# Kernel optimization log

Measured on AMD Instinct MI355X. Metric: run time of the kernel, lower is better.

Reference implementation:

```python
import jax, jax.numpy as jnp
import numpy as np

EPS_NORM = 1e-12   # torch F.normalize eps
EPS_TRIP = 1e-6    # torch pairwise_distance eps
MARGIN = 1.0

def _l2_normalize(x, axis=1):
    n = jnp.linalg.norm(x, axis=axis, keepdims=True)
    return x / jnp.maximum(n, EPS_NORM)

def setup_inputs() -> dict:
    key = jax.random.key(0)
    k1, k2 = jax.random.split(key)
    bs, m, d = 32768, 2048, 256
    query = jax.random.normal(k1, (bs, d), dtype=jnp.float32)
    memory = jax.random.normal(k2, (m, d), dtype=jnp.float32)
    return {"query": query, "memory": memory}

def reference(query, memory):
    m, d = memory.shape
    q = _l2_normalize(query, axis=1)                      # [bs, d]
    score = jnp.matmul(q, memory.T)                       # [bs, m]
    sfx_score_query = jax.nn.softmax(score, axis=0)       # softmax over batch
    sfx_score_memory = jax.nn.softmax(score, axis=1)      # softmax over slots

    # --- update (note: original passes sfx_score_query for BOTH score args) ---
    max_idx = jnp.argmax(sfx_score_query, axis=1)         # [bs] topk(k=1) over dim=1
    colmax = jnp.max(sfx_score_query, axis=0)             # [m]
    sel = jnp.take_along_axis(sfx_score_query, max_idx[:, None], axis=1)[:, 0]  # score[j, max_idx[j]]
    w = sel / colmax[max_idx]                              # [bs]
    # vectorized form of the per-slot gather/weighted-sum loop (segment-sum)
    query_update = jax.ops.segment_sum(w[:, None] * q, max_idx, num_segments=m)  # [m, d]
    updated_memory = jax.lax.stop_gradient(_l2_normalize(query_update + memory, axis=1))

    # --- read (uses ORIGINAL memory in the train path) ---
    concat_memory = jnp.matmul(jax.lax.stop_gradient(sfx_score_memory), memory)  # [bs, d]
    update_query = jnp.concatenate([q, concat_memory], axis=1)                   # [bs, 2d]

    # --- losses (computed from sfx_score_memory as intended) ---
    top2_vals, top2_idx = jax.lax.top_k(sfx_score_memory, 2)
    pos = jax.lax.stop_gradient(memory[top2_idx[:, 0]])   # [bs, d]
    neg = jax.lax.stop_gradient(memory[top2_idx[:, 1]])   # [bs, d]
    gathering_loss = jnp.mean((q - pos) ** 2)
    d_pos = jnp.linalg.norm(q - pos + EPS_TRIP, axis=1)
    d_neg = jnp.linalg.norm(q - neg + EPS_TRIP, axis=1)
    spreading_loss = jnp.mean(jnp.maximum(d_pos - d_neg + MARGIN, 0.0))

    return (update_query, updated_memory, sfx_score_query, sfx_score_memory,
            gathering_loss, spreading_loss)
```

## Files before the change

kernel.cpp:

```cpp
#include <hip/hip_runtime.h>
#include <hip/hip_bf16.h>
#include <cstddef>
#include <cstdint>

#define BS 32768
#define MSLOT 2048
#define D 256
#define NCHUNK 256

typedef _Float16 f16;
typedef _Float16 f16x8 __attribute__((ext_vector_type(8)));
typedef float f32x4 __attribute__((ext_vector_type(4)));

__device__ __forceinline__ void lds_cp16(void* dst, const void* src) {
    __builtin_amdgcn_global_load_lds(
        (const __attribute__((address_space(1))) void*)src,
        (__attribute__((address_space(3))) void*)dst, 16, 0, 0);
}

__device__ __forceinline__ void top2_merge(float& a0, int& ai0, float& a1, int& ai1,
                                           float b0, int bi0, float b1, int bi1)
{
    bool bt = (b0 > a0) || (b0 == a0 && bi0 < ai0);
    float n0, n1; int ni0, ni1;
    if (bt) {
        n0 = b0; ni0 = bi0;
        bool s2 = (b1 > a0) || (b1 == a0 && bi1 < ai0);
        n1 = s2 ? b1 : a0; ni1 = s2 ? bi1 : ai0;
    } else {
        n0 = a0; ni0 = ai0;
        bool s2 = (b0 > a1) || (b0 == a1 && bi0 < ai1);
        n1 = s2 ? b0 : a1; ni1 = s2 ? bi0 : ai1;
    }
    a0 = n0; ai0 = ni0; a1 = n1; ai1 = ni1;
}

__global__ __launch_bounds__(256) void k_prepq(const float* __restrict__ query,
                                               float* __restrict__ out0,
                                               f16* __restrict__ qh, f16* __restrict__ ql)
{
    __shared__ float sbuf[4];
    const int i = blockIdx.x, t = threadIdx.x;
    float v = query[(size_t)i * D + t];
    float ss = v * v;
#pragma unroll
    for (int off = 32; off; off >>= 1) ss += __shfl_xor(ss, off, 64);
    if ((t & 63) == 0) sbuf[t >> 6] = ss;
    __syncthreads();
    float tot = (sbuf[0] + sbuf[1]) + (sbuf[2] + sbuf[3]);
    float n = fmaxf(sqrtf(tot), 1e-12f);
    float qv = v / n;
    out0[(size_t)i * (2 * D) + t] = qv;
    float qs = qv * 256.0f;
    f16 h = (f16)qs;
    f16 lo = (f16)(qs - (float)h);
    qh[(size_t)i * D + t] = h;
    ql[(size_t)i * D + t] = lo;
}

__global__ __launch_bounds__(256) void k_prepm(const float* __restrict__ memory,
                                               f16* __restrict__ mh, f16* __restrict__ ml,
                                               f16* __restrict__ memT)
{
    const int j = blockIdx.x, t = threadIdx.x;
    float m = memory[(size_t)j * D + t];
    f16 h = (f16)m;
    f16 lo = (f16)(m - (float)h);
    mh[(size_t)j * D + t] = h;
    ml[(size_t)j * D + t] = lo;
    memT[(size_t)t * MSLOT + j] = h;
}

__global__ __launch_bounds__(256) void k_score(const f16* __restrict__ qh, const f16* __restrict__ ql,
                                               const f16* __restrict__ mh, const f16* __restrict__ ml,
                                               float* __restrict__ out2,
                                               float* __restrict__ colpart)
{
    __shared__ __align__(16) f16 Ah[4096], Al[4096], Bh[4096], Bl[4096];
    __shared__ float sepM[4][4][16], sepS[4][4][16];
    const int t = threadIdx.x;
    const int l = t & 63, w = t >> 6;
    const int wr = w >> 1, wc = w & 1;
    const int lk = l >> 4, lm = l & 15;
    const int i0 = blockIdx.y * 128, j0 = blockIdx.x * 128;

    f32x4 acc[4][4] = {};

    for (int ks = 0; ks < 8; ++ks) {
        const int k0 = ks * 32;
#pragma unroll
        for (int c = 0; c < 2; ++c) {
            int s = c * 256 + t;
            int r = s >> 2, cc = s & 3;
            int scc = cc ^ ((r >> 1) & 3);
            size_t aoff = (size_t)(i0 + r) * D + k0 + scc * 8;
            size_t boff = (size_t)(j0 + r) * D + k0 + scc * 8;
            lds_cp16(&Ah[s * 8], qh + aoff);
            lds_cp16(&Al[s * 8], ql + aoff);
            lds_cp16(&Bh[s * 8], mh + boff);
            lds_cp16(&Bl[s * 8], ml + boff);
        }
        __syncthreads();
        f16x8 a_h[4], a_l[4], b_h[4], b_l[4];
#pragma unroll
        for (int m = 0; m < 4; ++m) {
            int r = wr * 64 + m * 16 + lm;
            int off = r * 64 + ((lk ^ ((r >> 1) & 3)) << 4);
            a_h[m] = *(const f16x8*)((const char*)Ah + off);
            a_l[m] = *(const f16x8*)((const char*)Al + off);
        }
#pragma unroll
        for (int n = 0; n < 4; ++n) {
            int r = wc * 64 + n * 16 + lm;
            int off = r * 64 + ((lk ^ ((r >> 1) & 3)) << 4);
            b_h[n] = *(const f16x8*)((const char*)Bh + off);
            b_l[n] = *(const f16x8*)((const char*)Bl + off);
        }
#pragma unroll
        for (int m = 0; m < 4; ++m)
#pragma unroll
            for (int n = 0; n < 4; ++n) {
                acc[m][n] = __builtin_amdgcn_mfma_f32_16x16x32_f16(a_h[m], b_h[n], acc[m][n], 0, 0, 0);
                acc[m][n] = __builtin_amdgcn_mfma_f32_16x16x32_f16(a_h[m], b_l[n], acc[m][n], 0, 0, 0);
                acc[m][n] = __builtin_amdgcn_mfma_f32_16x16x32_f16(a_l[m], b_h[n], acc[m][n], 0, 0, 0);
            }
        __syncthreads();
    }

    const float sc = 1.0f / 256.0f;
#pragma unroll
    for (int m = 0; m < 4; ++m)
#pragma unroll
        for (int n = 0; n < 4; ++n)
            acc[m][n] *= sc;

#pragma unroll
    for (int m = 0; m < 4; ++m) {
        int row = i0 + wr * 64 + m * 16 + lk * 4;
#pragma unroll
        for (int n = 0; n < 4; ++n) {
            int col = j0 + wc * 64 + n * 16 + lm;
#pragma unroll
            for (int r = 0; r < 4; ++r)
                out2[(size_t)(row + r) * MSLOT + col] = acc[m][n][r];
        }
    }

    float cm[4], cs[4];
#pragma unroll
    for (int n = 0; n < 4; ++n) {
        float mx = -INFINITY;
#pragma unroll
        for (int m = 0; m < 4; ++m)
#pragma unroll
            for (int r = 0; r < 4; ++r) mx = fmaxf(mx, acc[m][n][r]);
        float sm = 0.0f;
#pragma unroll
        for (int m = 0; m < 4; ++m)
#pragma unroll
            for (int r = 0; r < 4; ++r) sm += __expf(acc[m][n][r] - mx);
#pragma unroll
        for (int off = 16; off <= 32; off <<= 1) {
            float om = __shfl_xor(mx, off, 64);
            float os = __shfl_xor(sm, off, 64);
            float nm = fmaxf(mx, om);
            sm = sm * __expf(mx - nm) + os * __expf(om - nm);
            mx = nm;
        }
        cm[n] = mx; cs[n] = sm;
    }
    if (l < 16) {
#pragma unroll
        for (int n = 0; n < 4; ++n) { sepM[w][n][l] = cm[n]; sepS[w][n][l] = cs[n]; }
    }
    __syncthreads();
    if (w < 2 && l < 16) {
#pragma unroll
        for (int n = 0; n < 4; ++n) {
            float m1 = sepM[w][n][l], s1 = sepS[w][n][l];
            float m2 = sepM[w + 2][n][l], s2 = sepS[w + 2][n][l];
            float nm = fmaxf(m1, m2);
            float ns = s1 * __expf(m1 - nm) + s2 * __expf(m2 - nm);
            int col = j0 + w * 64 + n * 16 + l;
            size_t o = ((size_t)blockIdx.y * MSLOT + col) * 2;
            colpart[o + 0] = nm;
            colpart[o + 1] = ns;
        }
    }
}

__global__ __launch_bounds__(256) void k_colmerge(const float* __restrict__ colpart,
                                                  float* __restrict__ colM,
                                                  float* __restrict__ colSinv,
                                                  float* __restrict__ colC)
{
    const int col = blockIdx.x * 256 + threadIdx.x;
    float m = -INFINITY, s = 0.0f;
    for (int c = 0; c < NCHUNK; ++c) {
        size_t o = ((size_t)c * MSLOT + col) * 2;
        float pm = colpart[o + 0], ps = colpart[o + 1];
        float nm = fmaxf(m, pm);
        s = s * __expf(m - nm) + ps * __expf(pm - nm);
        m = nm;
    }
    colM[col] = m;
    colSinv[col] = 1.0f / s;
    colC[col] = m + __logf(s);
}

__global__ __launch_bounds__(256) void k_rowtrans(float* __restrict__ sq,
                                                  float* __restrict__ sm,
                                                  const float* __restrict__ colM,
                                                  const float* __restrict__ colSinv,
                                                  const float* __restrict__ colC,
                                                  const float* __restrict__ out0,
                                                  const float* __restrict__ memory,
                                                  int* __restrict__ jstarA, float* __restrict__ wA,
                                                  float* __restrict__ gpart, float* __restrict__ spart)
{
    __shared__ float swm[4], sws[4];
    __shared__ float st0v[4], st1v[4]; __shared__ int st0i[4], st1i[4];
    __shared__ float sav[4], sar[4];  __shared__ int sai[4];
    __shared__ float sg[4], sdp[4], sdn[4];

    const int i = blockIdx.x, t = threadIdx.x;
    const int l = t & 63, w = t >> 6;
    float* row = sq + (size_t)i * MSLOT;
    float v[8];
#pragma unroll
    for (int k = 0; k < 8; ++k) v[k] = row[t + k * 256];

    float lmx = v[0];
#pragma unroll
    for (int k = 1; k < 8; ++k) lmx = fmaxf(lmx, v[k]);
#pragma unroll
    for (int off = 32; off; off >>= 1) lmx = fmaxf(lmx, __shfl_xor(lmx, off, 64));
    if (l == 0) swm[w] = lmx;
    __syncthreads();
    const float rm = fmaxf(fmaxf(swm[0], swm[1]), fmaxf(swm[2], swm[3]));

    float ls = 0.0f;
#pragma unroll
    for (int k = 0; k < 8; ++k) ls += __expf(v[k] - rm);

    float v0 = -INFINITY, v1 = -INFINITY; int i0 = 0x7fffffff, i1 = 0x7fffffff;
#pragma unroll
    for (int k = 0; k < 8; ++k) {
        int idx = t + k * 256; float cv = v[k];
        if (cv > v0)      { v1 = v0; i1 = i0; v0 = cv; i0 = idx; }
        else if (cv > v1) { v1 = cv; i1 = idx; }
    }

    float av = -INFINITY, araw = 0.0f; int ai = 0x7fffffff;
#pragma unroll
    for (int k = 0; k < 8; ++k) {
        int idx = t + k * 256;
        float x = v[k] - colC[idx];
        if (x > av || (x == av && idx < ai)) { av = x; ai = idx; araw = v[k]; }
    }

#pragma unroll
    for (int off = 32; off; off >>= 1) ls += __shfl_xor(ls, off, 64);
#pragma unroll
    for (int off = 1; off < 64; off <<= 1) {
        float b0 = __shfl_xor(v0, off, 64), b1 = __shfl_xor(v1, off, 64);
        int  bi0 = __shfl_xor(i0, off, 64), bi1 = __shfl_xor(i1, off, 64);
        top2_merge(v0, i0, v1, i1, b0, bi0, b1, bi1);
    }
#pragma unroll
    for (int off = 1; off < 64; off <<= 1) {
        float ov = __shfl_xor(av, off, 64), oraw = __shfl_xor(araw, off, 64);
        int   oi = __shfl_xor(ai, off, 64);
        if (ov > av || (ov == av && oi < ai)) { av = ov; ai = oi; araw = oraw; }
    }
    if (l == 0) {
        sws[w] = ls;
        st0v[w] = v0; st0i[w] = i0; st1v[w] = v1; st1i[w] = i1;
        sav[w] = av; sai[w] = ai; sar[w] = araw;
    }
    __syncthreads();

    const float rs = (sws[0] + sws[1]) + (sws[2] + sws[3]);
    const float rsinv = 1.0f / rs;

    float T0 = -INFINITY, T1 = -INFINITY; int I0 = 0x7fffffff, I1 = 0x7fffffff;
#pragma unroll
    for (int ww = 0; ww < 4; ++ww)
        top2_merge(T0, I0, T1, I1, st0v[ww], st0i[ww], st1v[ww], st1i[ww]);

    float AV = -INFINITY, AR = 0.0f; int AI = 0x7fffffff;
#pragma unroll
    for (int ww = 0; ww < 4; ++ww) {
        if (sav[ww] > AV || (sav[ww] == AV && sai[ww] < AI)) { AV = sav[ww]; AI = sai[ww]; AR = sar[ww]; }
    }

    float qv = out0[(size_t)i * (2 * D) + t];
    float pv = memory[(size_t)I0 * D + t];
    float nv = memory[(size_t)I1 * D + t];
    float dq = qv - pv;
    float g  = dq * dq;
    float dp = dq + 1e-6f;          dp *= dp;
    float dn = (qv - nv) + 1e-6f;   dn *= dn;
#pragma unroll
    for (int off = 32; off; off >>= 1) {
        g  += __shfl_xor(g, off, 64);
        dp += __shfl_xor(dp, off, 64);
        dn += __shfl_xor(dn, off, 64);
    }
    if (l == 0) { sg[w] = g; sdp[w] = dp; sdn[w] = dn; }
    __syncthreads();
    if (t == 0) {
        float gs  = (sg[0] + sg[1]) + (sg[2] + sg[3]);
        float dps = (sdp[0] + sdp[1]) + (sdp[2] + sdp[3]);
        float dns = (sdn[0] + sdn[1]) + (sdn[2] + sdn[3]);
        gpart[i] = gs;
        spart[i] = fmaxf(sqrtf(dps) - sqrtf(dns) + 1.0f, 0.0f);
        jstarA[i] = AI;
        wA[i] = __expf(AR - colM[AI]);
    }

#pragma unroll
    for (int k = 0; k < 8; ++k) {
        int j = t + k * 256;
        row[j] = __expf(v[k] - colM[j]) * colSinv[j];
        sm[(size_t)i * MSLOT + j] = __expf(v[k] - rm) * rsinv;
    }
}

__global__ __launch_bounds__(256) void k_scatter(const float* __restrict__ out0,
                                                 const int* __restrict__ jstarA,
                                                 const float* __restrict__ wA,
                                                 float* __restrict__ qupd)
{
    const int i = blockIdx.x, t = threadIdx.x;
    const int j = jstarA[i];
    const float wv = wA[i];
    unsafeAtomicAdd(&qupd[(size_t)j * D + t], wv * out0[(size_t)i * (2 * D) + t]);
}

__global__ __launch_bounds__(256) void k_updmem(const float* __restrict__ qupd,
                                                const float* __restrict__ memory,
                                                float* __restrict__ out1)
{
    __shared__ float sbuf[4];
    const int j = blockIdx.x, t = threadIdx.x;
    float v = qupd[(size_t)j * D + t] + memory[(size_t)j * D + t];
    float ss = v * v;
#pragma unroll
    for (int off = 32; off; off >>= 1) ss += __shfl_xor(ss, off, 64);
    if ((t & 63) == 0) sbuf[t >> 6] = ss;
    __syncthreads();
    float tot = (sbuf[0] + sbuf[1]) + (sbuf[2] + sbuf[3]);
    float n = fmaxf(sqrtf(tot), 1e-12f);
    out1[(size_t)j * D + t] = v / n;
}

__global__ __launch_bounds__(256) void k_concat(const float* __restrict__ P,
                                                const f16* __restrict__ memT,
                                                float* __restrict__ out0)
{
    __shared__ __align__(16) f16 As[2][4096 / 2];
    __shared__ __align__(16) f16 Bs[2][8192];
    const int t = threadIdx.x;
    const int l = t & 63, w = t >> 6;
    const int lk = l >> 4, lm = l & 15;
    const int i0 = blockIdx.x * 64;

    const int ar = t >> 2, acm = t & 3;
    const int aslot = acm ^ ((ar >> 1) & 3);

    f32x4 acc[4][4] = {};
    float4 pa, pb;

    {
        const float4* ap = (const float4*)(P + (size_t)(i0 + ar) * MSLOT + acm * 8);
        pa = ap[0]; pb = ap[1];
#pragma unroll
        for (int c = 0; c < 4; ++c) {
            int s = c * 256 + t;
            int n = s >> 2, cc = s & 3;
            int scc = cc ^ ((n >> 1) & 3);
            lds_cp16(&Bs[0][s * 8], memT + (size_t)n * MSLOT + scc * 8);
        }
        f16x8 h;
        h[0] = (f16)pa.x; h[1] = (f16)pa.y; h[2] = (f16)pa.z; h[3] = (f16)pa.w;
        h[4] = (f16)pb.x; h[5] = (f16)pb.y; h[6] = (f16)pb.z; h[7] = (f16)pb.w;
        *(f16x8*)((char*)As[0] + ar * 64 + (aslot << 4)) = h;
        __syncthreads();
    }

    for (int ks = 0; ks < 64; ++ks) {
        const int cur = ks & 1, nxt = cur ^ 1;
        if (ks < 63) {
            const int k0 = (ks + 1) * 32;
            const float4* ap = (const float4*)(P + (size_t)(i0 + ar) * MSLOT + k0 + acm * 8);
            pa = ap[0]; pb = ap[1];
#pragma unroll
            for (int c = 0; c < 4; ++c) {
                int s = c * 256 + t;
                int n = s >> 2, cc = s & 3;
                int scc = cc ^ ((n >> 1) & 3);
                lds_cp16(&Bs[nxt][s * 8], memT + (size_t)n * MSLOT + k0 + scc * 8);
            }
        }
        f16x8 af[4], bf[4];
#pragma unroll
        for (int m = 0; m < 4; ++m) {
            int r = m * 16 + lm;
            int off = r * 64 + ((lk ^ ((r >> 1) & 3)) << 4);
            af[m] = *(const f16x8*)((const char*)As[cur] + off);
        }
#pragma unroll
        for (int n = 0; n < 4; ++n) {
            int r = w * 64 + n * 16 + lm;
            int off = r * 64 + ((lk ^ ((r >> 1) & 3)) << 4);
            bf[n] = *(const f16x8*)((const char*)Bs[cur] + off);
        }
#pragma unroll
        for (int m = 0; m < 4; ++m)
#pragma unroll
            for (int n = 0; n < 4; ++n)
                acc[m][n] = __builtin_amdgcn_mfma_f32_16x16x32_f16(af[m], bf[n], acc[m][n], 0, 0, 0);

        if (ks < 63) {
            f16x8 h;
            h[0] = (f16)pa.x; h[1] = (f16)pa.y; h[2] = (f16)pa.z; h[3] = (f16)pa.w;
            h[4] = (f16)pb.x; h[5] = (f16)pb.y; h[6] = (f16)pb.z; h[7] = (f16)pb.w;
            *(f16x8*)((char*)As[nxt] + ar * 64 + (aslot << 4)) = h;
        }
        __syncthreads();
    }

#pragma unroll
    for (int m = 0; m < 4; ++m) {
        int row = i0 + m * 16 + lk * 4;
#pragma unroll
        for (int n = 0; n < 4; ++n) {
            int col = w * 64 + n * 16 + lm;
#pragma unroll
            for (int r = 0; r < 4; ++r)
                out0[(size_t)(row + r) * (2 * D) + D + col] = acc[m][n][r];
        }
    }
}

__global__ __launch_bounds__(256) void k_losses(const float* __restrict__ gpart,
                                                const float* __restrict__ spart,
                                                float* __restrict__ out45)
{
    __shared__ float sf[256];
    const int t = threadIdx.x;
    float g = 0.f, s = 0.f;
    for (int i = t; i < BS; i += 256) { g += gpart[i]; s += spart[i]; }
    sf[t] = g; __syncthreads();
    for (int off = 128; off; off >>= 1) { if (t < off) sf[t] += sf[t + off]; __syncthreads(); }
    float gt = sf[0]; __syncthreads();
    sf[t] = s; __syncthreads();
    for (int off = 128; off; off >>= 1) { if (t < off) sf[t] += sf[t + off]; __syncthreads(); }
    float st = sf[0];
    if (t == 0) {
        out45[0] = gt / (float)((size_t)BS * D);
        out45[1] = st / (float)BS;
    }
}

extern "C" void kernel_launch(void* const* d_in, const int* in_sizes, int n_in,
                              void* d_out, int out_size, void* d_ws, size_t ws_size,
                              hipStream_t stream)
{
    const float* query  = (const float*)d_in[0];
    const float* memory = (const float*)d_in[1];

    float* out  = (float*)d_out;
    float* out0 = out;
    float* out1 = out0 + (size_t)BS * 2 * D;
    float* out2 = out1 + (size_t)MSLOT * D;
    float* out3 = out2 + (size_t)BS * MSLOT;
    float* out45 = out3 + (size_t)BS * MSLOT;

    f16* qh   = (f16*)d_ws;
    f16* ql   = qh + (size_t)BS * D;
    f16* mh   = ql + (size_t)BS * D;
    f16* ml   = mh + (size_t)MSLOT * D;
    f16* memT = ml + (size_t)MSLOT * D;
    float* colpart = (float*)(memT + (size_t)D * MSLOT);
    float* colM    = colpart + (size_t)NCHUNK * MSLOT * 2;
    float* colSinv = colM + MSLOT;
    float* colC    = colSinv + MSLOT;
    float* wA      = colC + MSLOT;
    int*   jstarA  = (int*)(wA + BS);
    float* gpart   = (float*)(jstarA + BS);
    float* spart   = gpart + BS;
    float* qupd    = spart + BS;

    k_prepq<<<BS, 256, 0, stream>>>(query, out0, qh, ql);
    k_prepm<<<MSLOT, 256, 0, stream>>>(memory, mh, ml, memT);

    k_score<<<dim3(MSLOT / 128, BS / 128), 256, 0, stream>>>(qh, ql, mh, ml, out2, colpart);

    k_colmerge<<<MSLOT / 256, 256, 0, stream>>>(colpart, colM, colSinv, colC);

    k_rowtrans<<<BS, 256, 0, stream>>>(out2, out3, colM, colSinv, colC, out0, memory,
                                       jstarA, wA, gpart, spart);

    hipMemsetAsync(qupd, 0, (size_t)MSLOT * D * sizeof(float), stream);
    k_scatter<<<BS, 256, 0, stream>>>(out0, jstarA, wA, qupd);
    k_updmem<<<MSLOT, 256, 0, stream>>>(qupd, memory, out1);

    k_concat<<<BS / 64, 256, 0, stream>>>(out3, memT, out0);

    k_losses<<<1, 256, 0, stream>>>(gpart, spart, out45);
}
```

Measured before the change: 612.4 us.

## Double-buffer score GEMM, vectorize rowtrans, emit f16 probs for concat GEMM

Double-buffers the LDS tiles in the score GEMM so global loads overlap MFMA work. Vectorizes k_rowtrans loads and stores with a contiguous per-thread column layout and makes it also write an f16 copy of the row softmax. k_concat then reads that copy directly via LDS async copies, with a 128-row tile. The qupd memset is folded into k_prepm, and k_scatter reads the f16 hi/lo query halves instead of the fp32 output. The extra f16 probability buffer adds write traffic and workspace, and argmax tie-breaking now relies on ascending index order within each thread.

```diff
diff --git a/kernel.cpp b/kernel.cpp
--- a/kernel.cpp
+++ b/kernel.cpp
@@ -60,7 +60,8 @@
 
 __global__ __launch_bounds__(256) void k_prepm(const float* __restrict__ memory,
                                                f16* __restrict__ mh, f16* __restrict__ ml,
-                                               f16* __restrict__ memT)
+                                               f16* __restrict__ memT,
+                                               float* __restrict__ qupd)
 {
     const int j = blockIdx.x, t = threadIdx.x;
     float m = memory[(size_t)j * D + t];
@@ -69,6 +70,7 @@
     mh[(size_t)j * D + t] = h;
     ml[(size_t)j * D + t] = lo;
     memT[(size_t)t * MSLOT + j] = h;
+    qupd[(size_t)j * D + t] = 0.0f;
 }
 
 __global__ __launch_bounds__(256) void k_score(const f16* __restrict__ qh, const f16* __restrict__ ql,
@@ -76,7 +78,7 @@
                                                float* __restrict__ out2,
                                                float* __restrict__ colpart)
 {
-    __shared__ __align__(16) f16 Ah[4096], Al[4096], Bh[4096], Bl[4096];
+    __shared__ __align__(16) f16 Ah[2][4096], Al[2][4096], Bh[2][4096], Bl[2][4096];
     __shared__ float sepM[4][4][16], sepS[4][4][16];
     const int t = threadIdx.x;
     const int l = t & 63, w = t >> 6;
@@ -86,35 +88,43 @@
 
     f32x4 acc[4][4] = {};
 
+#define STAGE_SCORE(buf, k0)                                                     \
+    {                                                                            \
+        _Pragma("unroll")                                                        \
+        for (int c = 0; c < 2; ++c) {                                            \
+            int s = c * 256 + t;                                                 \
+            int r = s >> 2, cc = s & 3;                                          \
+            int scc = cc ^ ((r >> 1) & 3);                                       \
+            size_t aoff = (size_t)(i0 + r) * D + (k0) + scc * 8;                 \
+            size_t boff = (size_t)(j0 + r) * D + (k0) + scc * 8;                 \
+            lds_cp16(&Ah[buf][s * 8], qh + aoff);                                \
+            lds_cp16(&Al[buf][s * 8], ql + aoff);                                \
+            lds_cp16(&Bh[buf][s * 8], mh + boff);                                \
+            lds_cp16(&Bl[buf][s * 8], ml + boff);                                \
+        }                                                                        \
+    }
+
+    STAGE_SCORE(0, 0);
+    __syncthreads();
+
     for (int ks = 0; ks < 8; ++ks) {
-        const int k0 = ks * 32;
-#pragma unroll
-        for (int c = 0; c < 2; ++c) {
-            int s = c * 256 + t;
-            int r = s >> 2, cc = s & 3;
-            int scc = cc ^ ((r >> 1) & 3);
-            size_t aoff = (size_t)(i0 + r) * D + k0 + scc * 8;
-            size_t boff = (size_t)(j0 + r) * D + k0 + scc * 8;
-            lds_cp16(&Ah[s * 8], qh + aoff);
-            lds_cp16(&Al[s * 8], ql + aoff);
-            lds_cp16(&Bh[s * 8], mh + boff);
-            lds_cp16(&Bl[s * 8], ml + boff);
-        }
-        __syncthreads();
+        const int cur = ks & 1;
+        if (ks < 7) STAGE_SCORE(cur ^ 1, (ks + 1) * 32);
+
         f16x8 a_h[4], a_l[4], b_h[4], b_l[4];
 #pragma unroll
         for (int m = 0; m < 4; ++m) {
             int r = wr * 64 + m * 16 + lm;
             int off = r * 64 + ((lk ^ ((r >> 1) & 3)) << 4);
-            a_h[m] = *(const f16x8*)((const char*)Ah + off);
-            a_l[m] = *(const f16x8*)((const char*)Al + off);
+            a_h[m] = *(const f16x8*)((const char*)Ah[cur] + off);
+            a_l[m] = *(const f16x8*)((const char*)Al[cur] + off);
         }
 #pragma unroll
         for (int n = 0; n < 4; ++n) {
             int r = wc * 64 + n * 16 + lm;
             int off = r * 64 + ((lk ^ ((r >> 1) & 3)) << 4);
-            b_h[n] = *(const f16x8*)((const char*)Bh + off);
-            b_l[n] = *(const f16x8*)((const char*)Bl + off);
+            b_h[n] = *(const f16x8*)((const char*)Bh[cur] + off);
+            b_l[n] = *(const f16x8*)((const char*)Bl[cur] + off);
         }
 #pragma unroll
         for (int m = 0; m < 4; ++m)
@@ -126,6 +136,7 @@
             }
         __syncthreads();
     }
+#undef STAGE_SCORE
 
     const float sc = 1.0f / 256.0f;
 #pragma unroll
@@ -210,6 +221,7 @@
 
 __global__ __launch_bounds__(256) void k_rowtrans(float* __restrict__ sq,
                                                   float* __restrict__ sm,
+                                                  f16* __restrict__ pf16,
                                                   const float* __restrict__ colM,
                                                   const float* __restrict__ colSinv,
                                                   const float* __restrict__ colC,
@@ -225,10 +237,29 @@
 
     const int i = blockIdx.x, t = threadIdx.x;
     const int l = t & 63, w = t >> 6;
+    const int jb = t * 8;
     float* row = sq + (size_t)i * MSLOT;
+
     float v[8];
-#pragma unroll
-    for (int k = 0; k < 8; ++k) v[k] = row[t + k * 256];
+    {
+        float4 va = *(const float4*)(row + jb);
+        float4 vb = *(const float4*)(row + jb + 4);
+        v[0] = va.x; v[1] = va.y; v[2] = va.z; v[3] = va.w;
+        v[4] = vb.x; v[5] = vb.y; v[6] = vb.z; v[7] = vb.w;
+    }
+    float cCv[8], cMv[8], cSv[8];
+    {
+        float4 a = *(const float4*)(colC + jb);
+        float4 b = *(const float4*)(colC + jb + 4);
+        cCv[0] = a.x; cCv[1] = a.y; cCv[2] = a.z; cCv[3] = a.w;
+        cCv[4] = b.x; cCv[5] = b.y; cCv[6] = b.z; cCv[7] = b.w;
+        a = *(const float4*)(colM + jb); b = *(const float4*)(colM + jb + 4);
+        cMv[0] = a.x; cMv[1] = a.y; cMv[2] = a.z; cMv[3] = a.w;
+        cMv[4] = b.x; cMv[5] = b.y; cMv[6] = b.z; cMv[7] = b.w;
+        a = *(const float4*)(colSinv + jb); b = *(const float4*)(colSinv + jb + 4);
+        cSv[0] = a.x; cSv[1] = a.y; cSv[2] = a.z; cSv[3] = a.w;
+        cSv[4] = b.x; cSv[5] = b.y; cSv[6] = b.z; cSv[7] = b.w;
+    }
 
     float lmx = v[0];
 #pragma unroll
@@ -246,7 +277,7 @@
     float v0 = -INFINITY, v1 = -INFINITY; int i0 = 0x7fffffff, i1 = 0x7fffffff;
 #pragma unroll
     for (int k = 0; k < 8; ++k) {
-        int idx = t + k * 256; float cv = v[k];
+        int idx = jb + k; float cv = v[k];
         if (cv > v0)      { v1 = v0; i1 = i0; v0 = cv; i0 = idx; }
         else if (cv > v1) { v1 = cv; i1 = idx; }
     }
@@ -254,9 +285,9 @@
     float av = -INFINITY, araw = 0.0f; int ai = 0x7fffffff;
 #pragma unroll
     for (int k = 0; k < 8; ++k) {
-        int idx = t + k * 256;
-        float x = v[k] - colC[idx];
-        if (x > av || (x == av && idx < ai)) { av = x; ai = idx; araw = v[k]; }
+        int idx = jb + k;
+        float x = v[k] - cCv[k];
+        if (x > av) { av = x; ai = idx; araw = v[k]; }
     }
 
 #pragma unroll
@@ -319,23 +350,35 @@
         wA[i] = __expf(AR - colM[AI]);
     }
 
+    float oq[8], om[8];
 #pragma unroll
     for (int k = 0; k < 8; ++k) {
-        int j = t + k * 256;
-        row[j] = __expf(v[k] - colM[j]) * colSinv[j];
-        sm[(size_t)i * MSLOT + j] = __expf(v[k] - rm) * rsinv;
-    }
-}
-
-__global__ __launch_bounds__(256) void k_scatter(const float* __restrict__ out0,
+        oq[k] = __expf(v[k] - cMv[k]) * cSv[k];
+        om[k] = __expf(v[k] - rm) * rsinv;
+    }
+    float4 q0 = {oq[0], oq[1], oq[2], oq[3]}, q1 = {oq[4], oq[5], oq[6], oq[7]};
+    float4 m0 = {om[0], om[1], om[2], om[3]}, m1 = {om[4], om[5], om[6], om[7]};
+    *(float4*)(row + jb) = q0;
+    *(float4*)(row + jb + 4) = q1;
+    *(float4*)(sm + (size_t)i * MSLOT + jb) = m0;
+    *(float4*)(sm + (size_t)i * MSLOT + jb + 4) = m1;
+    f16x8 h;
+#pragma unroll
+    for (int k = 0; k < 8; ++k) h[k] = (f16)om[k];
+    *(f16x8*)(pf16 + (size_t)i * MSLOT + jb) = h;
+}
+
+__global__ __launch_bounds__(256) void k_scatter(const f16* __restrict__ qh,
+                                                 const f16* __restrict__ ql,
                                                  const int* __restrict__ jstarA,
                                                  const float* __restrict__ wA,
                                                  float* __restrict__ qupd)
 {
     const int i = blockIdx.x, t = threadIdx.x;
     const int j = jstarA[i];
-    const float wv = wA[i];
-    unsafeAtomicAdd(&qupd[(size_t)j * D + t], wv * out0[(size_t)i * (2 * D) + t]);
+    const float wv = wA[i] * (1.0f / 256.0f);
+    float qv = (float)qh[(size_t)i * D + t] + (float)ql[(size_t)i * D + t];
+    unsafeAtomicAdd(&qupd[(size_t)j * D + t], wv * qv);
 }
 
 __global__ __launch_bounds__(256) void k_updmem(const float* __restrict__ qupd,
@@ -355,88 +398,75 @@
     out1[(size_t)j * D + t] = v / n;
 }
 
-__global__ __launch_bounds__(256) void k_concat(const float* __restrict__ P,
+__global__ __launch_bounds__(256) void k_concat(const f16* __restrict__ P,
                                                 const f16* __restrict__ memT,
                                                 float* __restrict__ out0)
 {
-    __shared__ __align__(16) f16 As[2][4096 / 2];
+    __shared__ __align__(16) f16 As[2][4096];
     __shared__ __align__(16) f16 Bs[2][8192];
     const int t = threadIdx.x;
     const int l = t & 63, w = t >> 6;
     const int lk = l >> 4, lm = l & 15;
-    const int i0 = blockIdx.x * 64;
-
-    const int ar = t >> 2, acm = t & 3;
-    const int aslot = acm ^ ((ar >> 1) & 3);
-
-    f32x4 acc[4][4] = {};
-    float4 pa, pb;
-
-    {
-        const float4* ap = (const float4*)(P + (size_t)(i0 + ar) * MSLOT + acm * 8);
-        pa = ap[0]; pb = ap[1];
-#pragma unroll
-        for (int c = 0; c < 4; ++c) {
-            int s = c * 256 + t;
-            int n = s >> 2, cc = s & 3;
-            int scc = cc ^ ((n >> 1) & 3);
-            lds_cp16(&Bs[0][s * 8], memT + (size_t)n * MSLOT + scc * 8);
-        }
-        f16x8 h;
-        h[0] = (f16)pa.x; h[1] = (f16)pa.y; h[2] = (f16)pa.z; h[3] = (f16)pa.w;
-        h[4] = (f16)pb.x; h[5] = (f16)pb.y; h[6] = (f16)pb.z; h[7] = (f16)pb.w;
-        *(f16x8*)((char*)As[0] + ar * 64 + (aslot << 4)) = h;
-        __syncthreads();
-    }
+    const int i0 = blockIdx.x * 128;
+
+#define STAGE_CC(buf, k0)                                                        \
+    {                                                                            \
+        _Pragma("unroll")                                                        \
+        for (int c = 0; c < 2; ++c) {                                            \
+            int s = c * 256 + t;                                                 \
+            int r = s >> 2, cc = s & 3;                                          \
+            int scc = cc ^ ((r >> 1) & 3);                                       \
+            lds_cp16(&As[buf][s * 8], P + (size_t)(i0 + r) * MSLOT + (k0) + scc * 8); \
+        }                                                                        \
+        _Pragma("unroll")                                                        \
+        for (int c = 0; c < 4; ++c) {                                            \
+            int s = c * 256 + t;                                                 \
+            int n = s >> 2, cc = s & 3;                                          \
+            int scc = cc ^ ((n >> 1) & 3);                                       \
+            lds_cp16(&Bs[buf][s * 8], memT + (size_t)n * MSLOT + (k0) + scc * 8); \
+        }                                                                        \
+    }
+
+    f32x4 acc[2][16] = {};
+    STAGE_CC(0, 0);
+    __syncthreads();
 
     for (int ks = 0; ks < 64; ++ks) {
-        const int cur = ks & 1, nxt = cur ^ 1;
-        if (ks < 63) {
-            const int k0 = (ks + 1) * 32;
-            const float4* ap = (const float4*)(P + (size_t)(i0 + ar) * MSLOT + k0 + acm * 8);
-            pa = ap[0]; pb = ap[1];
-#pragma unroll
-            for (int c = 0; c < 4; ++c) {
-                int s = c * 256 + t;
-                int n = s >> 2, cc = s & 3;
-                int scc = cc ^ ((n >> 1) & 3);
-                lds_cp16(&Bs[nxt][s * 8], memT + (size_t)n * MSLOT + k0 + scc * 8);
-            }
-        }
-        f16x8 af[4], bf[4];
-#pragma unroll
-        for (int m = 0; m < 4; ++m) {
-            int r = m * 16 + lm;
+        const int cur = ks & 1;
+        if (ks < 63) STAGE_CC(cur ^ 1, (ks + 1) * 32);
+
+        f16x8 af[2];
+#pragma unroll
+        for (int m = 0; m < 2; ++m) {
+            int r = w * 32 + m * 16 + lm;
             int off = r * 64 + ((lk ^ ((r >> 1) & 3)) << 4);
             af[m] = *(const f16x8*)((const char*)As[cur] + off);
         }
 #pragma unroll
-        for (int n = 0; n < 4; ++n) {
-            int r = w * 64 + n * 16 + lm;
-            int off = r * 64 + ((lk ^ ((r >> 1) & 3)) << 4);
-            bf[n] = *(const f16x8*)((const char*)Bs[cur] + off);
-        }
-#pragma unroll
-        for (int m = 0; m < 4; ++m)
-#pragma unroll
-            for (int n = 0; n < 4; ++n)
-                acc[m][n] = __builtin_amdgcn_mfma_f32_16x16x32_f16(af[m], bf[n], acc[m][n], 0, 0, 0);
-
-        if (ks < 63) {
-            f16x8 h;
-            h[0] = (f16)pa.x; h[1] = (f16)pa.y; h[2] = (f16)pa.z; h[3] = (f16)pa.w;
-            h[4] = (f16)pb.x; h[5] = (f16)pb.y; h[6] = (f16)pb.z; h[7] = (f16)pb.w;
-            *(f16x8*)((char*)As[nxt] + ar * 64 + (aslot << 4)) = h;
+        for (int hh = 0; hh < 2; ++hh) {
+            f16x8 bf[8];
+#pragma unroll
+            for (int n = 0; n < 8; ++n) {
+                int r = (hh * 8 + n) * 16 + lm;
+                int off = r * 64 + ((lk ^ ((r >> 1) & 3)) << 4);
+                bf[n] = *(const f16x8*)((const char*)Bs[cur] + off);
+            }
+#pragma unroll
+            for (int m = 0; m < 2; ++m)
+#pragma unroll
+                for (int n = 0; n < 8; ++n)
+                    acc[m][hh * 8 + n] = __builtin_amdgcn_mfma_f32_16x16x32_f16(af[m], bf[n], acc[m][hh * 8 + n], 0, 0, 0);
         }
         __syncthreads();
     }
-
-#pragma unroll
-    for (int m = 0; m < 4; ++m) {
-        int row = i0 + m * 16 + lk * 4;
-#pragma unroll
-        for (int n = 0; n < 4; ++n) {
-            int col = w * 64 + n * 16 + lm;
+#undef STAGE_CC
+
+#pragma unroll
+    for (int m = 0; m < 2; ++m) {
+        int row = i0 + w * 32 + m * 16 + lk * 4;
+#pragma unroll
+        for (int n = 0; n < 16; ++n) {
+            int col = n * 16 + lm;
 #pragma unroll
             for (int r = 0; r < 4; ++r)
                 out0[(size_t)(row + r) * (2 * D) + D + col] = acc[m][n][r];
@@ -483,7 +513,8 @@
     f16* mh   = ql + (size_t)BS * D;
     f16* ml   = mh + (size_t)MSLOT * D;
     f16* memT = ml + (size_t)MSLOT * D;
-    float* colpart = (float*)(memT + (size_t)D * MSLOT);
+    f16* pf16 = memT + (size_t)D * MSLOT;
+    float* colpart = (float*)(pf16 + (size_t)BS * MSLOT);
     float* colM    = colpart + (size_t)NCHUNK * MSLOT * 2;
     float* colSinv = colM + MSLOT;
     float* colC    = colSinv + MSLOT;
@@ -494,20 +525,19 @@
     float* qupd    = spart + BS;
 
     k_prepq<<<BS, 256, 0, stream>>>(query, out0, qh, ql);
-    k_prepm<<<MSLOT, 256, 0, stream>>>(memory, mh, ml, memT);
+    k_prepm<<<MSLOT, 256, 0, stream>>>(memory, mh, ml, memT, qupd);
 
     k_score<<<dim3(MSLOT / 128, BS / 128), 256, 0, stream>>>(qh, ql, mh, ml, out2, colpart);
 
     k_colmerge<<<MSLOT / 256, 256, 0, stream>>>(colpart, colM, colSinv, colC);
 
-    k_rowtrans<<<BS, 256, 0, stream>>>(out2, out3, colM, colSinv, colC, out0, memory,
+    k_rowtrans<<<BS, 256, 0, stream>>>(out2, out3, pf16, colM, colSinv, colC, out0, memory,
                                        jstarA, wA, gpart, spart);
 
-    hipMemsetAsync(qupd, 0, (size_t)MSLOT * D * sizeof(float), stream);
-    k_scatter<<<BS, 256, 0, stream>>>(out0, jstarA, wA, qupd);
+    k_scatter<<<BS, 256, 0, stream>>>(qh, ql, jstarA, wA, qupd);
     k_updmem<<<MSLOT, 256, 0, stream>>>(qupd, memory, out1);
 
-    k_concat<<<BS / 64, 256, 0, stream>>>(out3, memT, out0);
+    k_concat<<<BS / 128, 256, 0, stream>>>(pf16, memT, out0);
 
     k_losses<<<1, 256, 0, stream>>>(gpart, spart, out45);
 }
```

Measured after the change: 640.9 us. +4.6%, slower.
